# Kernel optimization log

Hardware: AMD Instinct MI355X
Metric: run time of the kernel (lower is better)

The kernel has to match this reference:

```python
import jax, jax.numpy as jnp
import numpy as np

NUM_HEADS = 2
ROPE_BASE = 10000.0


def _rope_tables(seq_len, head_dim, dtype):
    # inv_freq over even indices of head_dim
    inv_freq = 1.0 / (ROPE_BASE ** (jnp.arange(0, head_dim, 2, dtype=jnp.float32) / head_dim))
    t = jnp.arange(seq_len, dtype=jnp.float32)
    freqs = t[:, None] * inv_freq[None, :]            # (s, head_dim/2)
    emb = jnp.concatenate([freqs, freqs], axis=-1)    # (s, head_dim)
    return jnp.cos(emb).astype(dtype), jnp.sin(emb).astype(dtype)


def _apply_rotation(x_bsd, cos, sin):
    # x_bsd: (b, s, h*d); chunk in half along last dim (h=2 -> halves == head_dim)
    x1, x2 = jnp.split(x_bsd, 2, axis=-1)
    return jnp.concatenate([x1 * cos - x2 * sin, x2 * cos + x1 * sin], axis=-1)


def setup_inputs() -> dict:
    key = jax.random.key(0)
    k1, k2, k3, k4 = jax.random.split(key, 4)
    b, s, dim = 4, 2048, 2048
    x = jax.random.normal(k1, (b, s, dim), dtype=jnp.float32)
    wqkv = jax.random.normal(k2, (dim, 3 * dim), dtype=jnp.float32) * (dim ** -0.5)
    wout = jax.random.normal(k3, (dim, dim), dtype=jnp.float32) * (dim ** -0.5)
    bout = jax.random.normal(k4, (dim,), dtype=jnp.float32) * 0.01
    return {"x": x, "wqkv": wqkv, "wout": wout, "bout": bout}


def reference(x, wqkv, wout, bout):
    b, s, dim = x.shape
    h = NUM_HEADS
    d = dim // h
    scale = d ** -0.5

    qkv = x @ wqkv                                    # (b, s, 3*dim)
    qkv = qkv.reshape(b, s, 3, h, d).transpose(2, 0, 3, 1, 4)  # (3, b, h, s, d)
    q, k, v = qkv[0], qkv[1], qkv[2]                  # (b, h, s, d)

    # RoPE applied on (b, s, h*d) layout, exactly as source
    cos, sin = _rope_tables(s, d, x.dtype)            # (s, d) each
    q_flat = q.transpose(0, 2, 1, 3).reshape(b, s, h * d)
    k_flat = k.transpose(0, 2, 1, 3).reshape(b, s, h * d)
    q = _apply_rotation(q_flat, cos, sin).reshape(b, s, h, d).transpose(0, 2, 1, 3)
    k = _apply_rotation(k_flat, cos, sin).reshape(b, s, h, d).transpose(0, 2, 1, 3)

    scores = jnp.einsum('bhid,bhjd->bhij', q, k) * scale
    attn = jax.nn.softmax(scores, axis=-1)
    out = jnp.einsum('bhij,bhjd->bhid', attn, v)      # (b, h, s, d)
    out = out.transpose(0, 2, 1, 3).reshape(b, s, dim)
    return out @ wout + bout
```

## Files before the change

kernel.cpp:

```cpp
#include <hip/hip_runtime.h>
#include <hip/hip_fp16.h>

typedef __attribute__((ext_vector_type(4))) float f32x4;
typedef __attribute__((ext_vector_type(8))) _Float16 f16x8;
typedef __attribute__((ext_vector_type(4))) _Float16 f16x4;

__device__ __forceinline__ void gload_lds16(const void* gp, void* lp) {
    __builtin_amdgcn_global_load_lds(
        (const __attribute__((address_space(1))) void*)gp,
        (__attribute__((address_space(3))) void*)lp, 16, 0, 0);
}

__global__ void rope_tables_k(float* __restrict__ cosT, float* __restrict__ sinT) {
    int idx = blockIdx.x * 256 + threadIdx.x;
    int s = idx >> 9, j = idx & 511;
    float invf = exp2f(-13.287712379549449f * (float)j * (1.0f / 512.0f));
    float ang = (float)s * invf;
    float sn, cs;
    sincosf(ang, &sn, &cs);
    cosT[idx] = cs;
    sinT[idx] = sn;
}

__global__ void f32_to_f16_vec(const float* __restrict__ in, _Float16* __restrict__ out) {
    long i = ((long)blockIdx.x * 256 + threadIdx.x) * 4;
    f32x4 v = *(const f32x4*)(in + i);
    f16x4 h;
#pragma unroll
    for (int e = 0; e < 4; ++e) h[e] = (_Float16)v[e];
    *(f16x4*)(out + i) = h;
}

__global__ void transpose_f32_to_f16(const float* __restrict__ in, _Float16* __restrict__ out,
                                     int R, int C) {
    __shared__ _Float16 tile[32][36];
    const int c0 = blockIdx.x * 32, r0 = blockIdx.y * 32;
    const int t = threadIdx.x;
    const int r = t >> 3, c4 = (t & 7) * 4;
    f32x4 v = *(const f32x4*)(in + (long)(r0 + r) * C + c0 + c4);
    f16x4 h;
#pragma unroll
    for (int e = 0; e < 4; ++e) h[e] = (_Float16)v[e];
    *(f16x4*)&tile[r][c4] = h;
    __syncthreads();
    const int oc = t >> 3, o4 = (t & 7) * 4;
    f16x4 o;
#pragma unroll
    for (int e = 0; e < 4; ++e) o[e] = tile[o4 + e][oc];
    *(f16x4*)(out + (long)(c0 + oc) * R + r0 + o4) = o;
}

__global__ void rope_inplace(_Float16* __restrict__ qkv, const float* __restrict__ cosT,
                             const float* __restrict__ sinT) {
    const int row = blockIdx.x;
    const int s = row & 2047;
    const int j0 = threadIdx.x * 4;
    _Float16* base = qkv + (long)row * 6144;
    f16x4 q0 = *(const f16x4*)(base + j0);
    f16x4 q1 = *(const f16x4*)(base + 1024 + j0);
    f16x4 k0 = *(const f16x4*)(base + 2048 + j0);
    f16x4 k1 = *(const f16x4*)(base + 3072 + j0);
    const int jj = j0 & 511;
    f32x4 cs = *(const f32x4*)(cosT + (long)s * 512 + jj);
    f32x4 sn = *(const f32x4*)(sinT + (long)s * 512 + jj);
    f16x4 oq0, oq1, ok0, ok1;
#pragma unroll
    for (int e = 0; e < 4; ++e) {
        float a = (float)q0[e], b = (float)q1[e];
        oq0[e] = (_Float16)(a * cs[e] - b * sn[e]);
        oq1[e] = (_Float16)(b * cs[e] + a * sn[e]);
        float c = (float)k0[e], d = (float)k1[e];
        ok0[e] = (_Float16)(c * cs[e] - d * sn[e]);
        ok1[e] = (_Float16)(d * cs[e] + c * sn[e]);
    }
    *(f16x4*)(base + j0) = oq0;
    *(f16x4*)(base + 1024 + j0) = oq1;
    *(f16x4*)(base + 2048 + j0) = ok0;
    *(f16x4*)(base + 3072 + j0) = ok1;
}

__global__ void v_transpose(const _Float16* __restrict__ qkv, _Float16* __restrict__ vT) {
    __shared__ _Float16 tile[32][36];
    const int z = blockIdx.z, b = z >> 1, h = z & 1;
    const int s0 = blockIdx.x * 32, d0 = blockIdx.y * 32;
    const int t = threadIdx.x;
    const int r = t >> 3, c4 = (t & 7) * 4;
    const _Float16* src = qkv + (long)(b * 2048 + s0 + r) * 6144 + 4096 + h * 1024 + d0 + c4;
    *(f16x4*)&tile[r][c4] = *(const f16x4*)src;
    __syncthreads();
    const int dr = t >> 3, sc = (t & 7) * 4;
    f16x4 o;
#pragma unroll
    for (int e = 0; e < 4; ++e) o[e] = tile[sc + e][dr];
    *(f16x4*)(vT + ((long)z * 1024 + d0 + dr) * 2048 + s0 + sc) = o;
}

__global__ __launch_bounds__(256) void softmax_rows_f32(float* __restrict__ S, float scale) {
    const int wid = threadIdx.x >> 6, lane = threadIdx.x & 63;
    const long row = (long)blockIdx.x * 4 + wid;
    float* rp = S + row * 2048;
    f32x4 v[8];
    float mx = -1e30f;
#pragma unroll
    for (int i = 0; i < 8; ++i) {
        v[i] = *(const f32x4*)(rp + (i * 64 + lane) * 4);
#pragma unroll
        for (int e = 0; e < 4; ++e) mx = fmaxf(mx, v[i][e]);
    }
#pragma unroll
    for (int o = 32; o > 0; o >>= 1) mx = fmaxf(mx, __shfl_xor(mx, o, 64));
    float sum = 0.f;
#pragma unroll
    for (int i = 0; i < 8; ++i)
#pragma unroll
        for (int e = 0; e < 4; ++e) {
            float p = __expf(scale * (v[i][e] - mx));
            v[i][e] = p; sum += p;
        }
#pragma unroll
    for (int o = 32; o > 0; o >>= 1) sum += __shfl_xor(sum, o, 64);
    float inv = 1.0f / sum;
    _Float16* wp = (_Float16*)S + row * 4096;
#pragma unroll
    for (int i = 0; i < 8; ++i) {
        f16x4 h;
#pragma unroll
        for (int e = 0; e < 4; ++e) h[e] = (_Float16)(v[i][e] * inv);
        *(f16x4*)(wp + (i * 64 + lane) * 4) = h;
    }
}

__global__ __launch_bounds__(256) void softmax_rows_f16(_Float16* __restrict__ S, float scale) {
    const int wid = threadIdx.x >> 6, lane = threadIdx.x & 63;
    const long row = (long)blockIdx.x * 4 + wid;
    _Float16* rp = S + row * 2048;
    f16x8 v[4];
    float f[32];
    float mx = -1e30f;
#pragma unroll
    for (int i = 0; i < 4; ++i) {
        v[i] = *(const f16x8*)(rp + i * 512 + lane * 8);
#pragma unroll
        for (int e = 0; e < 8; ++e) {
            f[i * 8 + e] = (float)v[i][e];
            mx = fmaxf(mx, f[i * 8 + e]);
        }
    }
#pragma unroll
    for (int o = 32; o > 0; o >>= 1) mx = fmaxf(mx, __shfl_xor(mx, o, 64));
    float sum = 0.f;
#pragma unroll
    for (int i = 0; i < 32; ++i) {
        float p = __expf(scale * (f[i] - mx));
        f[i] = p; sum += p;
    }
#pragma unroll
    for (int o = 32; o > 0; o >>= 1) sum += __shfl_xor(sum, o, 64);
    float inv = 1.0f / sum;
#pragma unroll
    for (int i = 0; i < 4; ++i) {
        f16x8 h;
#pragma unroll
        for (int e = 0; e < 8; ++e) h[e] = (_Float16)(f[i * 8 + e] * inv);
        *(f16x8*)(rp + i * 512 + lane * 8) = h;
    }
}

template <bool OUT_F16, bool BIAS>
__global__ __launch_bounds__(512, 2)
void gemm256(const _Float16* __restrict__ A, const _Float16* __restrict__ B,
             void* __restrict__ Cv, const float* __restrict__ bias,
             int K, int lda, int ldb, int ldc, int zmod,
             long a1, long a2, long b1, long b2, long c1, long c2) {
    __shared__ char lds[131072];
    const int z = blockIdx.z, zq = z / zmod, zr = z - zq * zmod;
    A += zq * a1 + zr * a2;
    B += zq * b1 + zr * b2;
    const long coff = zq * c1 + zr * c2;
    const int tm = blockIdx.y * 256, tn = blockIdx.x * 256;
    const int t = threadIdx.x;
    const int lane = t & 63, wid = t >> 6;
    const int wr = wid >> 2, wc = wid & 3;
    const int fr = lane & 15, kg = lane >> 4;

    const int strow = wid * 16 + (lane >> 3);
    const int stcol = ((lane & 7) ^ (lane >> 3)) * 8;
    const _Float16* gA = A + (long)(tm + strow) * lda + stcol;
    const _Float16* gB = B + (long)(tn + strow) * ldb + stcol;
    char* const ldsw = lds + wid * 2048;

    const int sw0 = 16 * ((0 * 4 + kg) ^ (fr & 7));
    const int sw1 = 16 * ((1 * 4 + kg) ^ (fr & 7));

    const int NT = K >> 6;
    f32x4 acc[8][4] = {};

    auto stageA = [&](int tt, int h) {
        const _Float16* s = gA + (long)(h * 128) * lda + tt * 64;
        char* d = ldsw + (tt & 1) * 65536 + h * 16384;
        gload_lds16(s, d);
        gload_lds16(s + (long)8 * lda, d + 1024);
    };
    auto stageB = [&](int tt, int h) {
        const _Float16* s = gB + (long)(h * 128) * ldb + tt * 64;
        char* d = ldsw + (tt & 1) * 65536 + 32768 + h * 16384;
        gload_lds16(s, d);
        gload_lds16(s + (long)8 * ldb, d + 1024);
    };

    stageB(0, 0); stageB(0, 1); stageA(0, 0); stageA(0, 1);
    stageB(1, 0); stageB(1, 1);
    asm volatile("s_waitcnt vmcnt(4)" ::: "memory");
    __builtin_amdgcn_s_barrier();

    f16x8 af[4][2], bf0[2][2], bf1[2][2];
    const int arow = (wr * 128 + fr) * 128;
    const int brow = 32768 + (wc * 64 + fr) * 128;

    for (int g = 0; g < NT; ++g) {
        const char* buf = lds + (g & 1) * 65536;
#pragma unroll
        for (int m = 0; m < 4; ++m) {
            af[m][0] = *(const f16x8*)(buf + arow + m * 2048 + sw0);
            af[m][1] = *(const f16x8*)(buf + arow + m * 2048 + sw1);
        }
#pragma unroll
        for (int n = 0; n < 2; ++n) {
            bf0[n][0] = *(const f16x8*)(buf + brow + n * 2048 + sw0);
            bf0[n][1] = *(const f16x8*)(buf + brow + n * 2048 + sw1);
        }
        if (g + 1 < NT) stageA(g + 1, 0);
        __builtin_amdgcn_s_barrier();
        __builtin_amdgcn_s_setprio(1);
#pragma unroll
        for (int m = 0; m < 4; ++m)
#pragma unroll
            for (int n = 0; n < 2; ++n)
#pragma unroll
                for (int k = 0; k < 2; ++k)
                    acc[m][n] = __builtin_amdgcn_mfma_f32_16x16x32_f16(af[m][k], bf0[n][k], acc[m][n], 0, 0, 0);
        __builtin_amdgcn_s_setprio(0);
        __builtin_amdgcn_s_barrier();
#pragma unroll
        for (int n = 0; n < 2; ++n) {
            bf1[n][0] = *(const f16x8*)(buf + brow + 4096 + n * 2048 + sw0);
            bf1[n][1] = *(const f16x8*)(buf + brow + 4096 + n * 2048 + sw1);
        }
        if (g + 1 < NT) stageA(g + 1, 1);
        __builtin_amdgcn_s_barrier();
        __builtin_amdgcn_s_setprio(1);
#pragma unroll
        for (int m = 0; m < 4; ++m)
#pragma unroll
            for (int n = 0; n < 2; ++n)
#pragma unroll
                for (int k = 0; k < 2; ++k)
                    acc[m][n + 2] = __builtin_amdgcn_mfma_f32_16x16x32_f16(af[m][k], bf1[n][k], acc[m][n + 2], 0, 0, 0);
        __builtin_amdgcn_s_setprio(0);
        __builtin_amdgcn_s_barrier();
#pragma unroll
        for (int m = 0; m < 4; ++m) {
            af[m][0] = *(const f16x8*)(buf + arow + 8192 + m * 2048 + sw0);
            af[m][1] = *(const f16x8*)(buf + arow + 8192 + m * 2048 + sw1);
        }
        if (g + 2 < NT) stageB(g + 2, 0);
        __builtin_amdgcn_s_barrier();
        __builtin_amdgcn_s_setprio(1);
#pragma unroll
        for (int m = 0; m < 4; ++m)
#pragma unroll
            for (int n = 0; n < 2; ++n)
#pragma unroll
                for (int k = 0; k < 2; ++k)
                    acc[m + 4][n + 2] = __builtin_amdgcn_mfma_f32_16x16x32_f16(af[m][k], bf1[n][k], acc[m + 4][n + 2], 0, 0, 0);
        __builtin_amdgcn_s_setprio(0);
        __builtin_amdgcn_s_barrier();
        if (g + 2 < NT) stageB(g + 2, 1);
        __builtin_amdgcn_s_barrier();
        __builtin_amdgcn_s_setprio(1);
#pragma unroll
        for (int m = 0; m < 4; ++m)
#pragma unroll
            for (int n = 0; n < 2; ++n)
#pragma unroll
                for (int k = 0; k < 2; ++k)
                    acc[m + 4][n] = __builtin_amdgcn_mfma_f32_16x16x32_f16(af[m][k], bf0[n][k], acc[m + 4][n], 0, 0, 0);
        __builtin_amdgcn_s_setprio(0);
        if (g + 2 < NT)      asm volatile("s_waitcnt vmcnt(4)" ::: "memory");
        else if (g + 1 < NT) asm volatile("s_waitcnt vmcnt(0)" ::: "memory");
        __builtin_amdgcn_s_barrier();
    }

    const int rb = tm + wr * 128 + (lane >> 4) * 4;
    const int cb = tn + wc * 64 + fr;
#pragma unroll
    for (int m = 0; m < 8; ++m) {
#pragma unroll
        for (int n = 0; n < 4; ++n) {
#pragma unroll
            for (int r = 0; r < 4; ++r) {
                float v = acc[m][n][r];
                const int row = rb + m * 16 + r;
                const int col = cb + n * 16;
                if (BIAS) v += bias[col];
                if (OUT_F16)
                    ((_Float16*)Cv)[coff + (long)row * ldc + col] = (_Float16)v;
                else
                    ((float*)Cv)[coff + (long)row * ldc + col] = v;
            }
        }
    }
}

extern "C" void kernel_launch(void* const* d_in, const int* in_sizes, int n_in,
                              void* d_out, int out_size, void* d_ws, size_t ws_size,
                              hipStream_t stream) {
    const float* x    = (const float*)d_in[0];
    const float* wqkv = (const float*)d_in[1];
    const float* wout = (const float*)d_in[2];
    const float* bout = (const float*)d_in[3];
    char* ws = (char*)d_ws;

    _Float16* qkv_h = (_Float16*)(ws);
    _Float16* x_h   = (_Float16*)(ws + 100663296);
    _Float16* wqkvT = (_Float16*)(ws + 134217728);
    _Float16* vT    = (_Float16*)(ws + 100663296);
    float*    cosT  = (float*)(ws + 100663296);
    float*    sinT  = (float*)(ws + 104857600);
    _Float16* woutT = (_Float16*)(ws);
    const bool batched = ws_size >= 234881024ULL;

    f32_to_f16_vec<<<dim3(16384), dim3(256), 0, stream>>>(x, x_h);
    transpose_f32_to_f16<<<dim3(192, 64), dim3(256), 0, stream>>>(wqkv, wqkvT, 2048, 6144);
    gemm256<true, false><<<dim3(24, 32, 1), dim3(512), 0, stream>>>(
        x_h, wqkvT, (void*)qkv_h, nullptr, 2048, 2048, 2048, 6144,
        1, 0L, 0L, 0L, 0L, 0L, 0L);
    rope_tables_k<<<dim3(4096), dim3(256), 0, stream>>>(cosT, sinT);
    rope_inplace<<<dim3(8192), dim3(256), 0, stream>>>(qkv_h, cosT, sinT);
    v_transpose<<<dim3(64, 32, 8), dim3(256), 0, stream>>>(qkv_h, vT);

    if (batched) {
        _Float16* S16  = (_Float16*)(ws + 134217728);
        _Float16* aout = (_Float16*)(ws + 201326592);
        gemm256<true, false><<<dim3(8, 8, 8), dim3(512), 0, stream>>>(
            qkv_h, qkv_h + 2048, (void*)S16, nullptr, 1024, 6144, 6144, 2048,
            2, 12582912L, 1024L, 12582912L, 1024L, 8388608L, 4194304L);
        softmax_rows_f16<<<dim3(4096), dim3(256), 0, stream>>>(S16, 0.03125f);
        gemm256<true, false><<<dim3(4, 8, 8), dim3(512), 0, stream>>>(
            S16, vT, (void*)aout, nullptr, 2048, 2048, 2048, 2048,
            2, 8388608L, 4194304L, 4194304L, 2097152L, 4194304L, 1024L);
        transpose_f32_to_f16<<<dim3(64, 64), dim3(256), 0, stream>>>(wout, woutT, 2048, 2048);
        gemm256<false, true><<<dim3(8, 32, 1), dim3(512), 0, stream>>>(
            aout, woutT, d_out, bout, 2048, 2048, 2048, 2048,
            1, 0L, 0L, 0L, 0L, 0L, 0L);
    } else {
        float*    S32  = (float*)(ws + 134217728);
        _Float16* aout = (_Float16*)(ws + 150994944);
        for (int z = 0; z < 8; ++z) {
            const _Float16* Az = qkv_h + (long)(z >> 1) * 12582912 + (z & 1) * 1024;
            gemm256<false, false><<<dim3(8, 8, 1), dim3(512), 0, stream>>>(
                Az, Az + 2048, (void*)S32, nullptr, 1024, 6144, 6144, 2048,
                1, 0L, 0L, 0L, 0L, 0L, 0L);
            softmax_rows_f32<<<dim3(512), dim3(256), 0, stream>>>(S32, 0.03125f);
            gemm256<true, false><<<dim3(4, 8, 1), dim3(512), 0, stream>>>(
                (const _Float16*)S32, vT + (long)z * 2097152,
                (void*)(aout + (long)(z >> 1) * 4194304 + (z & 1) * 1024), nullptr,
                2048, 4096, 2048, 2048, 1, 0L, 0L, 0L, 0L, 0L, 0L);
        }
        transpose_f32_to_f16<<<dim3(64, 64), dim3(256), 0, stream>>>(wout, woutT, 2048, 2048);
        gemm256<false, true><<<dim3(8, 32, 1), dim3(512), 0, stream>>>(
            aout, woutT, d_out, bout, 2048, 2048, 2048, 2048,
            1, 0L, 0L, 0L, 0L, 0L, 0L);
    }
}
```

Before: 520.1 us.

## Fuse exp into QK^T epilogue and row normalization into PV epilogue

The QK^T GEMM epilogue now writes exp(scale*s) directly as f16, so the softmax kernel shrinks to a read-only row-sum pass. The PV GEMM epilogue divides each output row by that sum. This drops one full read-modify-write pass over the score matrix. The cost is that the max subtraction is gone, so exp can overflow f16 for large scores, which is a numerical risk. GEMM barriers are also switched to inline-asm s_barrier with a memory clobber, and the batched path now needs slightly more workspace.

```diff
diff --git a/kernel.cpp b/kernel.cpp
--- a/kernel.cpp
+++ b/kernel.cpp
@@ -9,6 +9,10 @@
     __builtin_amdgcn_global_load_lds(
         (const __attribute__((address_space(1))) void*)gp,
         (__attribute__((address_space(3))) void*)lp, 16, 0, 0);
+}
+
+__device__ __forceinline__ void barrier_fenced() {
+    asm volatile("s_barrier" ::: "memory");
 }
 
 __global__ void rope_tables_k(float* __restrict__ cosT, float* __restrict__ sinT) {
@@ -130,46 +134,27 @@
     }
 }
 
-__global__ __launch_bounds__(256) void softmax_rows_f16(_Float16* __restrict__ S, float scale) {
+__global__ __launch_bounds__(256) void rowsum_f16(const _Float16* __restrict__ S,
+                                                  float* __restrict__ l) {
     const int wid = threadIdx.x >> 6, lane = threadIdx.x & 63;
     const long row = (long)blockIdx.x * 4 + wid;
-    _Float16* rp = S + row * 2048;
-    f16x8 v[4];
-    float f[32];
-    float mx = -1e30f;
+    const _Float16* rp = S + row * 2048;
+    float sum = 0.f;
 #pragma unroll
     for (int i = 0; i < 4; ++i) {
-        v[i] = *(const f16x8*)(rp + i * 512 + lane * 8);
-#pragma unroll
-        for (int e = 0; e < 8; ++e) {
-            f[i * 8 + e] = (float)v[i][e];
-            mx = fmaxf(mx, f[i * 8 + e]);
-        }
-    }
-#pragma unroll
-    for (int o = 32; o > 0; o >>= 1) mx = fmaxf(mx, __shfl_xor(mx, o, 64));
-    float sum = 0.f;
-#pragma unroll
-    for (int i = 0; i < 32; ++i) {
-        float p = __expf(scale * (f[i] - mx));
-        f[i] = p; sum += p;
+        f16x8 v = *(const f16x8*)(rp + i * 512 + lane * 8);
+#pragma unroll
+        for (int e = 0; e < 8; ++e) sum += (float)v[e];
     }
 #pragma unroll
     for (int o = 32; o > 0; o >>= 1) sum += __shfl_xor(sum, o, 64);
-    float inv = 1.0f / sum;
-#pragma unroll
-    for (int i = 0; i < 4; ++i) {
-        f16x8 h;
-#pragma unroll
-        for (int e = 0; e < 8; ++e) h[e] = (_Float16)(f[i * 8 + e] * inv);
-        *(f16x8*)(rp + i * 512 + lane * 8) = h;
-    }
-}
-
-template <bool OUT_F16, bool BIAS>
+    if (lane == 0) l[row] = sum;
+}
+
+template <int OMODE, bool BIAS>
 __global__ __launch_bounds__(512, 2)
 void gemm256(const _Float16* __restrict__ A, const _Float16* __restrict__ B,
-             void* __restrict__ Cv, const float* __restrict__ bias,
+             void* __restrict__ Cv, const float* __restrict__ aux, float scale,
              int K, int lda, int ldb, int ldc, int zmod,
              long a1, long a2, long b1, long b2, long c1, long c2) {
     __shared__ char lds[131072];
@@ -211,7 +196,7 @@
     stageB(0, 0); stageB(0, 1); stageA(0, 0); stageA(0, 1);
     stageB(1, 0); stageB(1, 1);
     asm volatile("s_waitcnt vmcnt(4)" ::: "memory");
-    __builtin_amdgcn_s_barrier();
+    barrier_fenced();
 
     f16x8 af[4][2], bf0[2][2], bf1[2][2];
     const int arow = (wr * 128 + fr) * 128;
@@ -230,7 +215,7 @@
             bf0[n][1] = *(const f16x8*)(buf + brow + n * 2048 + sw1);
         }
         if (g + 1 < NT) stageA(g + 1, 0);
-        __builtin_amdgcn_s_barrier();
+        barrier_fenced();
         __builtin_amdgcn_s_setprio(1);
 #pragma unroll
         for (int m = 0; m < 4; ++m)
@@ -240,14 +225,14 @@
                 for (int k = 0; k < 2; ++k)
                     acc[m][n] = __builtin_amdgcn_mfma_f32_16x16x32_f16(af[m][k], bf0[n][k], acc[m][n], 0, 0, 0);
         __builtin_amdgcn_s_setprio(0);
-        __builtin_amdgcn_s_barrier();
+        barrier_fenced();
 #pragma unroll
         for (int n = 0; n < 2; ++n) {
             bf1[n][0] = *(const f16x8*)(buf + brow + 4096 + n * 2048 + sw0);
             bf1[n][1] = *(const f16x8*)(buf + brow + 4096 + n * 2048 + sw1);
         }
         if (g + 1 < NT) stageA(g + 1, 1);
-        __builtin_amdgcn_s_barrier();
+        barrier_fenced();
         __builtin_amdgcn_s_setprio(1);
 #pragma unroll
         for (int m = 0; m < 4; ++m)
@@ -257,14 +242,14 @@
                 for (int k = 0; k < 2; ++k)
                     acc[m][n + 2] = __builtin_amdgcn_mfma_f32_16x16x32_f16(af[m][k], bf1[n][k], acc[m][n + 2], 0, 0, 0);
         __builtin_amdgcn_s_setprio(0);
-        __builtin_amdgcn_s_barrier();
+        barrier_fenced();
 #pragma unroll
         for (int m = 0; m < 4; ++m) {
             af[m][0] = *(const f16x8*)(buf + arow + 8192 + m * 2048 + sw0);
             af[m][1] = *(const f16x8*)(buf + arow + 8192 + m * 2048 + sw1);
         }
         if (g + 2 < NT) stageB(g + 2, 0);
-        __builtin_amdgcn_s_barrier();
+        barrier_fenced();
         __builtin_amdgcn_s_setprio(1);
 #pragma unroll
         for (int m = 0; m < 4; ++m)
@@ -274,9 +259,9 @@
                 for (int k = 0; k < 2; ++k)
                     acc[m + 4][n + 2] = __builtin_amdgcn_mfma_f32_16x16x32_f16(af[m][k], bf1[n][k], acc[m + 4][n + 2], 0, 0, 0);
         __builtin_amdgcn_s_setprio(0);
-        __builtin_amdgcn_s_barrier();
+        barrier_fenced();
         if (g + 2 < NT) stageB(g + 2, 1);
-        __builtin_amdgcn_s_barrier();
+        barrier_fenced();
         __builtin_amdgcn_s_setprio(1);
 #pragma unroll
         for (int m = 0; m < 4; ++m)
@@ -288,25 +273,31 @@
         __builtin_amdgcn_s_setprio(0);
         if (g + 2 < NT)      asm volatile("s_waitcnt vmcnt(4)" ::: "memory");
         else if (g + 1 < NT) asm volatile("s_waitcnt vmcnt(0)" ::: "memory");
-        __builtin_amdgcn_s_barrier();
+        barrier_fenced();
     }
 
     const int rb = tm + wr * 128 + (lane >> 4) * 4;
     const int cb = tn + wc * 64 + fr;
+    const float* auxz = (OMODE == 3) ? (aux + (long)z * 2048) : aux;
 #pragma unroll
     for (int m = 0; m < 8; ++m) {
 #pragma unroll
-        for (int n = 0; n < 4; ++n) {
-#pragma unroll
-            for (int r = 0; r < 4; ++r) {
+        for (int r = 0; r < 4; ++r) {
+            const int row = rb + m * 16 + r;
+            float inv = 1.0f;
+            if (OMODE == 3) inv = __builtin_amdgcn_rcpf(auxz[row]);
+#pragma unroll
+            for (int n = 0; n < 4; ++n) {
                 float v = acc[m][n][r];
-                const int row = rb + m * 16 + r;
                 const int col = cb + n * 16;
-                if (BIAS) v += bias[col];
-                if (OUT_F16)
+                if (BIAS) v += aux[col];
+                if (OMODE == 0) {
+                    ((float*)Cv)[coff + (long)row * ldc + col] = v;
+                } else {
+                    if (OMODE == 2) v = __expf(v * scale);
+                    if (OMODE == 3) v *= inv;
                     ((_Float16*)Cv)[coff + (long)row * ldc + col] = (_Float16)v;
-                else
-                    ((float*)Cv)[coff + (long)row * ldc + col] = v;
+                }
             }
         }
     }
@@ -328,12 +319,12 @@
     float*    cosT  = (float*)(ws + 100663296);
     float*    sinT  = (float*)(ws + 104857600);
     _Float16* woutT = (_Float16*)(ws);
-    const bool batched = ws_size >= 234881024ULL;
+    const bool batched = ws_size >= 234946560ULL;
 
     f32_to_f16_vec<<<dim3(16384), dim3(256), 0, stream>>>(x, x_h);
     transpose_f32_to_f16<<<dim3(192, 64), dim3(256), 0, stream>>>(wqkv, wqkvT, 2048, 6144);
-    gemm256<true, false><<<dim3(24, 32, 1), dim3(512), 0, stream>>>(
-        x_h, wqkvT, (void*)qkv_h, nullptr, 2048, 2048, 2048, 6144,
+    gemm256<1, false><<<dim3(24, 32, 1), dim3(512), 0, stream>>>(
+        x_h, wqkvT, (void*)qkv_h, nullptr, 0.f, 2048, 2048, 2048, 6144,
         1, 0L, 0L, 0L, 0L, 0L, 0L);
     rope_tables_k<<<dim3(4096), dim3(256), 0, stream>>>(cosT, sinT);
     rope_inplace<<<dim3(8192), dim3(256), 0, stream>>>(qkv_h, cosT, sinT);
@@ -342,34 +333,35 @@
     if (batched) {
         _Float16* S16  = (_Float16*)(ws + 134217728);
         _Float16* aout = (_Float16*)(ws + 201326592);
-        gemm256<true, false><<<dim3(8, 8, 8), dim3(512), 0, stream>>>(
-            qkv_h, qkv_h + 2048, (void*)S16, nullptr, 1024, 6144, 6144, 2048,
+        float*    lsum = (float*)(ws + 234881024);
+        gemm256<2, false><<<dim3(8, 8, 8), dim3(512), 0, stream>>>(
+            qkv_h, qkv_h + 2048, (void*)S16, nullptr, 0.03125f, 1024, 6144, 6144, 2048,
             2, 12582912L, 1024L, 12582912L, 1024L, 8388608L, 4194304L);
-        softmax_rows_f16<<<dim3(4096), dim3(256), 0, stream>>>(S16, 0.03125f);
-        gemm256<true, false><<<dim3(4, 8, 8), dim3(512), 0, stream>>>(
-            S16, vT, (void*)aout, nullptr, 2048, 2048, 2048, 2048,
+        rowsum_f16<<<dim3(4096), dim3(256), 0, stream>>>(S16, lsum);
+        gemm256<3, false><<<dim3(4, 8, 8), dim3(512), 0, stream>>>(
+            S16, vT, (void*)aout, lsum, 0.f, 2048, 2048, 2048, 2048,
             2, 8388608L, 4194304L, 4194304L, 2097152L, 4194304L, 1024L);
         transpose_f32_to_f16<<<dim3(64, 64), dim3(256), 0, stream>>>(wout, woutT, 2048, 2048);
-        gemm256<false, true><<<dim3(8, 32, 1), dim3(512), 0, stream>>>(
-            aout, woutT, d_out, bout, 2048, 2048, 2048, 2048,
+        gemm256<0, true><<<dim3(8, 32, 1), dim3(512), 0, stream>>>(
+            aout, woutT, d_out, bout, 0.f, 2048, 2048, 2048, 2048,
             1, 0L, 0L, 0L, 0L, 0L, 0L);
     } else {
         float*    S32  = (float*)(ws + 134217728);
         _Float16* aout = (_Float16*)(ws + 150994944);
         for (int z = 0; z < 8; ++z) {
             const _Float16* Az = qkv_h + (long)(z >> 1) * 12582912 + (z & 1) * 1024;
-            gemm256<false, false><<<dim3(8, 8, 1), dim3(512), 0, stream>>>(
-                Az, Az + 2048, (void*)S32, nullptr, 1024, 6144, 6144, 2048,
+            gemm256<0, false><<<dim3(8, 8, 1), dim3(512), 0, stream>>>(
+                Az, Az + 2048, (void*)S32, nullptr, 0.f, 1024, 6144, 6144, 2048,
                 1, 0L, 0L, 0L, 0L, 0L, 0L);
             softmax_rows_f32<<<dim3(512), dim3(256), 0, stream>>>(S32, 0.03125f);
-            gemm256<true, false><<<dim3(4, 8, 1), dim3(512), 0, stream>>>(
+            gemm256<1, false><<<dim3(4, 8, 1), dim3(512), 0, stream>>>(
                 (const _Float16*)S32, vT + (long)z * 2097152,
-                (void*)(aout + (long)(z >> 1) * 4194304 + (z & 1) * 1024), nullptr,
+                (void*)(aout + (long)(z >> 1) * 4194304 + (z & 1) * 1024), nullptr, 0.f,
                 2048, 4096, 2048, 2048, 1, 0L, 0L, 0L, 0L, 0L, 0L);
         }
         transpose_f32_to_f16<<<dim3(64, 64), dim3(256), 0, stream>>>(wout, woutT, 2048, 2048);
-        gemm256<false, true><<<dim3(8, 32, 1), dim3(512), 0, stream>>>(
-            aout, woutT, d_out, bout, 2048, 2048, 2048, 2048,
+        gemm256<0, true><<<dim3(8, 32, 1), dim3(512), 0, stream>>>(
+            aout, woutT, d_out, bout, 0.f, 2048, 2048, 2048, 2048,
             1, 0L, 0L, 0L, 0L, 0L, 0L);
     }
 }
```

New measurement: 510.5 us. Within noise of the previous version (-1.9%).
